# Kernel tuning notes

Measured on AMD Instinct MI355X. Metric: run time of the kernel, lower is better.

The kernel has to match this reference:

```python
import jax, jax.numpy as jnp
import numpy as np

B, C, H, W = 32, 512, 40, 40
NC = 20
STRIDE = 32
CONF_THRESH = 0.3
NMS_THRESH = 0.5


def setup_inputs() -> dict:
    key = jax.random.key(0)
    ks = jax.random.split(key, 7)
    # 0.02 scale on weights keeps sigmoid/exp in a realistic, non-saturated range
    return {
        "feat": jax.random.normal(ks[0], (B, C, H, W), dtype=jnp.float32),
        "w_obj": jax.random.normal(ks[1], (1, C), dtype=jnp.float32) * 0.02,
        "b_obj": jnp.zeros((1,), dtype=jnp.float32),
        "w_cls": jax.random.normal(ks[2], (NC, C), dtype=jnp.float32) * 0.02,
        "b_cls": jnp.zeros((NC,), dtype=jnp.float32),
        "w_reg": jax.random.normal(ks[3], (4, C), dtype=jnp.float32) * 0.02,
        "b_reg": jnp.zeros((4,), dtype=jnp.float32),
    }


def _pairwise_iou(b):  # b: [N,4] xyxy
    area = (b[:, 2] - b[:, 0]) * (b[:, 3] - b[:, 1])
    x1 = jnp.maximum(b[:, None, 0], b[None, :, 0])
    y1 = jnp.maximum(b[:, None, 1], b[None, :, 1])
    x2 = jnp.minimum(b[:, None, 2], b[None, :, 2])
    y2 = jnp.minimum(b[:, None, 3], b[None, :, 3])
    inter = jnp.maximum(x2 - x1, 0.0) * jnp.maximum(y2 - y1, 0.0)
    union = area[:, None] + area[None, :] - inter
    return inter / union


def _nms_single(boxes, scores, labels, conf_mask):
    # Greedy per-class NMS with fixed shapes (keep mask), matching the
    # original: suppression happens only among boxes of the same class
    # that pass conf_thresh, in descending score order.
    N = boxes.shape[0]
    order = jnp.argsort(-scores)
    b = boxes[order]
    l = labels[order]
    v = conf_mask[order]
    iou = _pairwise_iou(b)  # [N,N]
    idx = jnp.arange(N)
    later = idx[None, :] > idx[:, None]
    sup = (iou > NMS_THRESH) & (l[:, None] == l[None, :]) & later

    def body(i, keep):
        # if box i is still kept, suppress all later same-class overlaps
        return keep & ~(sup[i] & keep[i])

    keep_sorted = jax.lax.fori_loop(0, N, body, v)
    return jnp.zeros((N,), dtype=bool).at[order].set(keep_sorted)


def reference(feat, w_obj, b_obj, w_cls, b_cls, w_reg, b_reg):
    Bn, Cc, Hh, Ww = feat.shape
    N = Hh * Ww
    # permute(0,2,3,1).flatten(1,2) -> [B, H*W, C]
    x = feat.transpose(0, 2, 3, 1).reshape(Bn, N, Cc)
    # 1x1 convs == per-cell linear layers
    obj = jnp.einsum("bnc,oc->bno", x, w_obj) + b_obj  # [B,N,1]
    cls = jnp.einsum("bnc,oc->bno", x, w_cls) + b_cls  # [B,N,NC]
    reg = jnp.einsum("bnc,oc->bno", x, w_reg) + b_reg  # [B,N,4]
    # decode_boxes
    gy, gx = jnp.meshgrid(jnp.arange(Hh), jnp.arange(Ww), indexing="ij")
    grid = jnp.stack([gx, gy], axis=-1).reshape(-1, 2).astype(feat.dtype)  # [N,2]
    ctr = (jax.nn.sigmoid(reg[..., :2]) + grid) * STRIDE
    wh = jnp.exp(reg[..., 2:]) * STRIDE
    boxes = jnp.concatenate([ctr - wh * 0.5, ctr + wh * 0.5], axis=-1)  # [B,N,4]
    # scores = sqrt(sigmoid(obj) * sigmoid(cls)); per-cell best class
    sc = jnp.sqrt(jax.nn.sigmoid(obj) * jax.nn.sigmoid(cls))  # [B,N,NC]
    scores = sc.max(axis=-1)
    labels = jnp.argmax(sc, axis=-1)
    conf_mask = scores > CONF_THRESH
    keep = jax.vmap(_nms_single)(boxes, scores, labels, conf_mask)  # [B,N]
    out = jnp.concatenate(
        [jnp.where(keep[..., None], boxes, 0.0),
         jnp.where(keep, scores, 0.0)[..., None]],
        axis=-1,
    )  # [B,N,5]
    return out, labels, keep
```

## Files before the change

### kernel.cpp

```cpp
#include <hip/hip_runtime.h>
#include <stdint.h>
#include <stddef.h>

#define Bn 32
#define Cc 512
#define Hh 40
#define Ww 40
#define Npix 1600
#define NCx 20
#define NCELL (Bn*Npix)
#define CONF 0.3f
#define NMS_T 0.5f
#define NOUT 25
#define WSTRIDE 32

#define CB 64
#define BPI 25
#define NWAVE 4
#define CR (Cc/NWAVE)

#define WS_WPK    0
#define WS_BOXES  (WS_WPK + (size_t)Cc*WSTRIDE)
#define WS_SCORES (WS_BOXES + (size_t)NCELL*4)
#define WS_LABELS (WS_SCORES + (size_t)NCELL)

__device__ __forceinline__ float sigmoidf_(float x) {
    return 1.0f / (1.0f + expf(-x));
}

__global__ __launch_bounds__(64) void k0_pack(
    const float* __restrict__ w_obj, const float* __restrict__ w_cls,
    const float* __restrict__ w_reg, float* __restrict__ Wpk)
{
    int c = blockIdx.x * 64 + threadIdx.x;
    if (c < Cc) {
        float* row = Wpk + (size_t)c * WSTRIDE;
        row[0] = w_obj[c];
        #pragma unroll
        for (int o = 0; o < NCx; ++o) row[1 + o] = w_cls[o * Cc + c];
        #pragma unroll
        for (int o = 0; o < 4; ++o)   row[21 + o] = w_reg[o * Cc + c];
        row[25] = 0.f; row[26] = 0.f; row[27] = 0.f;
        row[28] = 0.f; row[29] = 0.f; row[30] = 0.f; row[31] = 0.f;
    }
}

__global__ __launch_bounds__(256) void k1_fused(
    const float* __restrict__ feat, const float* __restrict__ Wpk,
    const float* __restrict__ b_obj, const float* __restrict__ b_cls,
    const float* __restrict__ b_reg,
    float* __restrict__ out, float* __restrict__ ws_boxes,
    float* __restrict__ ws_scores, int* __restrict__ ws_labels)
{
    __shared__ float red[NOUT][CB][5];

    const int tid = threadIdx.x;
    const int w   = __builtin_amdgcn_readfirstlane(tid >> 6);
    const int l   = tid & 63;
    const int b   = blockIdx.x / BPI;
    const int j   = blockIdx.x % BPI;
    const int n0  = j * CB;

    float acc[NOUT];
    #pragma unroll
    for (int o = 0; o < NOUT; ++o) acc[o] = 0.f;

    const int cw0 = w * CR;
    {
        const float* fp  = feat + (size_t)b * (Cc * Npix) + (size_t)cw0 * Npix + (n0 + l);
        const float* wr0 = Wpk + (size_t)cw0 * WSTRIDE;
        #pragma unroll 4
        for (int cc = 0; cc < CR; ++cc) {
            float x = fp[(size_t)cc * Npix];
            const float4* wq = (const float4*)(wr0 + cc * WSTRIDE);
            #pragma unroll
            for (int q = 0; q < 6; ++q) {
                float4 wv = wq[q];
                const int ob = q * 4;
                acc[ob+0] = fmaf(x, wv.x, acc[ob+0]);
                acc[ob+1] = fmaf(x, wv.y, acc[ob+1]);
                acc[ob+2] = fmaf(x, wv.z, acc[ob+2]);
                acc[ob+3] = fmaf(x, wv.w, acc[ob+3]);
            }
            float4 wv6 = wq[6];
            acc[24] = fmaf(x, wv6.x, acc[24]);
        }
        #pragma unroll
        for (int o = 0; o < NOUT; ++o) red[o][l][w] = acc[o];
    }
    __syncthreads();

    if (tid < CB) {
        float v[NOUT];
        #pragma unroll
        for (int o = 0; o < NOUT; ++o) v[o] = red[o][tid][0];
        #pragma unroll
        for (int ch = 1; ch < NWAVE; ++ch) {
            #pragma unroll
            for (int o = 0; o < NOUT; ++o) v[o] += red[o][tid][ch];
        }

        float obj = v[0] + b_obj[0];
        float m = -1e30f; int label = 0;
        #pragma unroll
        for (int o = 0; o < NCx; ++o) {
            float cv = v[1 + o] + b_cls[o];
            if (cv > m) { m = cv; label = o; }
        }
        float r0 = v[21] + b_reg[0], r1 = v[22] + b_reg[1];
        float r2 = v[23] + b_reg[2], r3 = v[24] + b_reg[3];

        int n = n0 + tid;
        int g = b * Npix + n;
        int gy = n / Ww, gx = n % Ww;
        float cx = (sigmoidf_(r0) + (float)gx) * 32.0f;
        float cy = (sigmoidf_(r1) + (float)gy) * 32.0f;
        float bw = expf(r2) * 32.0f;
        float bh = expf(r3) * 32.0f;
        float x1 = cx - bw * 0.5f, y1 = cy - bh * 0.5f;
        float x2 = cx + bw * 0.5f, y2 = cy + bh * 0.5f;
        float score = sqrtf(sigmoidf_(obj) * sigmoidf_(m));

        ((float4*)ws_boxes)[g] = make_float4(x1, y1, x2, y2);
        ws_scores[g] = score;
        ws_labels[g] = label;

        float* orow = out + (size_t)g * 5;
        orow[0] = 0.f; orow[1] = 0.f; orow[2] = 0.f; orow[3] = 0.f; orow[4] = 0.f;
        out[(size_t)NCELL * 5 + g] = (float)label;
        out[(size_t)NCELL * 6 + g] = 0.f;
    }
}

#define KSUP 320
#define WUMAX ((KSUP + 31) / 32)

__global__ __launch_bounds__(256) void k3_nms(
    const float4* __restrict__ ws_boxes, const float* __restrict__ ws_scores,
    const int* __restrict__ ws_labels, float* __restrict__ out)
{
    __shared__ unsigned int cnt;
    __shared__ unsigned long long keys[2048];
    __shared__ float bx1[Npix], by1[Npix], bx2[Npix], by2[Npix], bar[Npix];
    __shared__ unsigned int sup[KSUP * WUMAX];
    __shared__ unsigned int keepbits[WUMAX];

    const int tid = threadIdx.x;
    const int b   = blockIdx.x / NCx;
    const int cls = blockIdx.x % NCx;
    const int gbase = b * Npix;

    if (tid == 0) cnt = 0;
    __syncthreads();

    for (int n = tid; n < Npix; n += 256) {
        float s = ws_scores[gbase + n];
        if (s > CONF && ws_labels[gbase + n] == cls) {
            unsigned int pos = atomicAdd(&cnt, 1u);
            unsigned int sb = __float_as_uint(s);
            keys[pos] = ((unsigned long long)(~sb) << 32) | (unsigned int)n;
        }
    }
    __syncthreads();
    const int k = (int)cnt;
    if (k == 0) return;

    int M = 2; while (M < k) M <<= 1;
    for (int s = tid; s < M; s += 256) if (s >= k) keys[s] = ~0ull;
    __syncthreads();

    for (int sz = 2; sz <= M; sz <<= 1) {
        for (int st = sz >> 1; st > 0; st >>= 1) {
            for (int t = tid; t < M; t += 256) {
                int p = t ^ st;
                if (p > t) {
                    unsigned long long a = keys[t], c = keys[p];
                    bool up = ((t & sz) == 0);
                    if (up ? (a > c) : (a < c)) { keys[t] = c; keys[p] = a; }
                }
            }
            __syncthreads();
        }
    }

    for (int s = tid; s < k; s += 256) {
        int n = (int)(unsigned int)keys[s];
        float4 bx = ws_boxes[gbase + n];
        bx1[s] = bx.x; by1[s] = bx.y; bx2[s] = bx.z; by2[s] = bx.w;
        bar[s] = (bx.z - bx.x) * (bx.w - bx.y);
    }
    __syncthreads();

    if (k <= KSUP) {
        const int wu = (k + 31) >> 5;
        for (int t = tid; t < k * wu; t += 256) {
            int i = t / wu, w = t - (t / wu) * wu;
            unsigned int bits = 0;
            int j0 = w << 5;
            float xi1 = bx1[i], yi1 = by1[i], xi2 = bx2[i], yi2 = by2[i], ai = bar[i];
            for (int jj = 0; jj < 32; ++jj) {
                int j = j0 + jj;
                if (j > i && j < k) {
                    float xx1 = fmaxf(xi1, bx1[j]);
                    float yy1 = fmaxf(yi1, by1[j]);
                    float xx2 = fminf(xi2, bx2[j]);
                    float yy2 = fminf(yi2, by2[j]);
                    float inter = fmaxf(xx2 - xx1, 0.f) * fmaxf(yy2 - yy1, 0.f);
                    float uni = ai + bar[j] - inter;
                    if (inter / uni > NMS_T) bits |= (1u << jj);
                }
            }
            sup[i * wu + w] = bits;
        }
        if (tid < wu) {
            int rem = k - (tid << 5);
            keepbits[tid] = (rem >= 32) ? 0xFFFFFFFFu : ((1u << rem) - 1u);
        }
        __syncthreads();

        if (tid < 64) {
            for (int i = 0; i < k; ++i) {
                unsigned int cur = keepbits[i >> 5];
                if ((cur >> (i & 31)) & 1u) {
                    if (tid < wu) keepbits[tid] &= ~sup[i * wu + tid];
                }
            }
            unsigned int* keepF = sup;
            for (int s2 = tid; s2 < k; s2 += 64)
                keepF[s2] = (keepbits[s2 >> 5] >> (s2 & 31)) & 1u;
        }
        __syncthreads();
    } else {
        unsigned int* keepF = sup;
        for (int s = tid; s < k; s += 256) keepF[s] = 1u;
        __syncthreads();
        for (int i = 0; i < k; ++i) {
            __syncthreads();
            if (keepF[i]) {
                float xi1 = bx1[i], yi1 = by1[i], xi2 = bx2[i], yi2 = by2[i], ai = bar[i];
                for (int j = i + 1 + tid; j < k; j += 256) {
                    float xx1 = fmaxf(xi1, bx1[j]);
                    float yy1 = fmaxf(yi1, by1[j]);
                    float xx2 = fminf(xi2, bx2[j]);
                    float yy2 = fminf(yi2, by2[j]);
                    float inter = fmaxf(xx2 - xx1, 0.f) * fmaxf(yy2 - yy1, 0.f);
                    float uni = ai + bar[j] - inter;
                    if (inter / uni > NMS_T) keepF[j] = 0u;
                }
            }
        }
        __syncthreads();
    }

    unsigned int* keepF = sup;
    for (int s = tid; s < k; s += 256) {
        if (keepF[s]) {
            int n = (int)(unsigned int)keys[s];
            unsigned int sb = ~(unsigned int)(keys[s] >> 32);
            float sc = __uint_as_float(sb);
            float* orow = out + (size_t)(gbase + n) * 5;
            orow[0] = bx1[s]; orow[1] = by1[s];
            orow[2] = bx2[s]; orow[3] = by2[s];
            orow[4] = sc;
            out[(size_t)NCELL * 6 + gbase + n] = 1.0f;
        }
    }
}

extern "C" void kernel_launch(void* const* d_in, const int* in_sizes, int n_in,
                              void* d_out, int out_size, void* d_ws, size_t ws_size,
                              hipStream_t stream) {
    const float* feat  = (const float*)d_in[0];
    const float* w_obj = (const float*)d_in[1];
    const float* b_obj = (const float*)d_in[2];
    const float* w_cls = (const float*)d_in[3];
    const float* b_cls = (const float*)d_in[4];
    const float* w_reg = (const float*)d_in[5];
    const float* b_reg = (const float*)d_in[6];
    float* out = (float*)d_out;
    float* ws  = (float*)d_ws;

    float* Wpk    = ws + WS_WPK;
    float* boxes  = ws + WS_BOXES;
    float* scores = ws + WS_SCORES;
    int*   labels = (int*)(ws + WS_LABELS);

    k0_pack<<<(Cc + 63) / 64, 64, 0, stream>>>(w_obj, w_cls, w_reg, Wpk);
    k1_fused<<<Bn * BPI, 256, 0, stream>>>(feat, Wpk, b_obj, b_cls, b_reg,
                                           out, boxes, scores, labels);
    k3_nms<<<Bn * NCx, 256, 0, stream>>>((const float4*)boxes, scores, labels, out);
}
```

Baseline: 220.7 us.

## Preload all feature channels into registers and use output-major weight layout

The weight pack is changed from a per-channel row of 32 floats to an output-major [25][512] layout. The projection kernel now loads all 128 channel values for its pixel into registers up front, then computes the 25 outputs in five passes of five accumulators each. The shared reduction buffer is reordered to [wave][out][pixel]. The aim is to issue all feature loads at once for more memory-level parallelism, at the cost of heavy register pressure (128 values held), which may lower occupancy or cause spills.

```diff
diff --git a/kernel.cpp b/kernel.cpp
--- a/kernel.cpp
+++ b/kernel.cpp
@@ -12,15 +12,14 @@
 #define CONF 0.3f
 #define NMS_T 0.5f
 #define NOUT 25
-#define WSTRIDE 32
 
 #define CB 64
 #define BPI 25
 #define NWAVE 4
 #define CR (Cc/NWAVE)
 
-#define WS_WPK    0
-#define WS_BOXES  (WS_WPK + (size_t)Cc*WSTRIDE)
+#define WS_WT     0
+#define WS_BOXES  (WS_WT + (size_t)NOUT*Cc)
 #define WS_SCORES (WS_BOXES + (size_t)NCELL*4)
 #define WS_LABELS (WS_SCORES + (size_t)NCELL)
 
@@ -30,29 +29,26 @@
 
 __global__ __launch_bounds__(64) void k0_pack(
     const float* __restrict__ w_obj, const float* __restrict__ w_cls,
-    const float* __restrict__ w_reg, float* __restrict__ Wpk)
+    const float* __restrict__ w_reg, float* __restrict__ Wt)
 {
     int c = blockIdx.x * 64 + threadIdx.x;
     if (c < Cc) {
-        float* row = Wpk + (size_t)c * WSTRIDE;
-        row[0] = w_obj[c];
-        #pragma unroll
-        for (int o = 0; o < NCx; ++o) row[1 + o] = w_cls[o * Cc + c];
-        #pragma unroll
-        for (int o = 0; o < 4; ++o)   row[21 + o] = w_reg[o * Cc + c];
-        row[25] = 0.f; row[26] = 0.f; row[27] = 0.f;
-        row[28] = 0.f; row[29] = 0.f; row[30] = 0.f; row[31] = 0.f;
+        Wt[c] = w_obj[c];
+        #pragma unroll
+        for (int o = 0; o < NCx; ++o) Wt[(size_t)(1 + o) * Cc + c] = w_cls[o * Cc + c];
+        #pragma unroll
+        for (int o = 0; o < 4; ++o)   Wt[(size_t)(21 + o) * Cc + c] = w_reg[o * Cc + c];
     }
 }
 
 __global__ __launch_bounds__(256) void k1_fused(
-    const float* __restrict__ feat, const float* __restrict__ Wpk,
+    const float* __restrict__ feat, const float* __restrict__ Wt,
     const float* __restrict__ b_obj, const float* __restrict__ b_cls,
     const float* __restrict__ b_reg,
     float* __restrict__ out, float* __restrict__ ws_boxes,
     float* __restrict__ ws_scores, int* __restrict__ ws_labels)
 {
-    __shared__ float red[NOUT][CB][5];
+    __shared__ float red[NWAVE][NOUT][CB];
 
     const int tid = threadIdx.x;
     const int w   = __builtin_amdgcn_readfirstlane(tid >> 6);
@@ -61,43 +57,47 @@
     const int j   = blockIdx.x % BPI;
     const int n0  = j * CB;
 
-    float acc[NOUT];
-    #pragma unroll
-    for (int o = 0; o < NOUT; ++o) acc[o] = 0.f;
-
-    const int cw0 = w * CR;
     {
-        const float* fp  = feat + (size_t)b * (Cc * Npix) + (size_t)cw0 * Npix + (n0 + l);
-        const float* wr0 = Wpk + (size_t)cw0 * WSTRIDE;
-        #pragma unroll 4
-        for (int cc = 0; cc < CR; ++cc) {
-            float x = fp[(size_t)cc * Npix];
-            const float4* wq = (const float4*)(wr0 + cc * WSTRIDE);
+        const float* fp = feat + (size_t)b * (Cc * Npix) + (size_t)(w * CR) * Npix + (n0 + l);
+        float x[CR];
+        #pragma unroll
+        for (int cc = 0; cc < CR; ++cc) x[cc] = fp[(size_t)cc * Npix];
+
+        const float* wt0 = Wt + w * CR;
+        #pragma unroll
+        for (int q = 0; q < 5; ++q) {
+            const float* w0 = wt0 + (size_t)(5 * q + 0) * Cc;
+            const float* w1 = wt0 + (size_t)(5 * q + 1) * Cc;
+            const float* w2 = wt0 + (size_t)(5 * q + 2) * Cc;
+            const float* w3 = wt0 + (size_t)(5 * q + 3) * Cc;
+            const float* w4 = wt0 + (size_t)(5 * q + 4) * Cc;
+            float a0 = 0.f, a1 = 0.f, a2 = 0.f, a3 = 0.f, a4 = 0.f;
             #pragma unroll
-            for (int q = 0; q < 6; ++q) {
-                float4 wv = wq[q];
-                const int ob = q * 4;
-                acc[ob+0] = fmaf(x, wv.x, acc[ob+0]);
-                acc[ob+1] = fmaf(x, wv.y, acc[ob+1]);
-                acc[ob+2] = fmaf(x, wv.z, acc[ob+2]);
-                acc[ob+3] = fmaf(x, wv.w, acc[ob+3]);
-            }
-            float4 wv6 = wq[6];
-            acc[24] = fmaf(x, wv6.x, acc[24]);
-        }
-        #pragma unroll
-        for (int o = 0; o < NOUT; ++o) red[o][l][w] = acc[o];
+            for (int cc = 0; cc < CR; ++cc) {
+                float xv = x[cc];
+                a0 = fmaf(xv, w0[cc], a0);
+                a1 = fmaf(xv, w1[cc], a1);
+                a2 = fmaf(xv, w2[cc], a2);
+                a3 = fmaf(xv, w3[cc], a3);
+                a4 = fmaf(xv, w4[cc], a4);
+            }
+            red[w][5 * q + 0][l] = a0;
+            red[w][5 * q + 1][l] = a1;
+            red[w][5 * q + 2][l] = a2;
+            red[w][5 * q + 3][l] = a3;
+            red[w][5 * q + 4][l] = a4;
+        }
     }
     __syncthreads();
 
     if (tid < CB) {
         float v[NOUT];
         #pragma unroll
-        for (int o = 0; o < NOUT; ++o) v[o] = red[o][tid][0];
+        for (int o = 0; o < NOUT; ++o) v[o] = red[0][o][tid];
         #pragma unroll
         for (int ch = 1; ch < NWAVE; ++ch) {
             #pragma unroll
-            for (int o = 0; o < NOUT; ++o) v[o] += red[o][tid][ch];
+            for (int o = 0; o < NOUT; ++o) v[o] += red[ch][o][tid];
         }
 
         float obj = v[0] + b_obj[0];
@@ -280,13 +280,13 @@
     float* out = (float*)d_out;
     float* ws  = (float*)d_ws;
 
-    float* Wpk    = ws + WS_WPK;
+    float* Wt     = ws + WS_WT;
     float* boxes  = ws + WS_BOXES;
     float* scores = ws + WS_SCORES;
     int*   labels = (int*)(ws + WS_LABELS);
 
-    k0_pack<<<(Cc + 63) / 64, 64, 0, stream>>>(w_obj, w_cls, w_reg, Wpk);
-    k1_fused<<<Bn * BPI, 256, 0, stream>>>(feat, Wpk, b_obj, b_cls, b_reg,
+    k0_pack<<<(Cc + 63) / 64, 64, 0, stream>>>(w_obj, w_cls, w_reg, Wt);
+    k1_fused<<<Bn * BPI, 256, 0, stream>>>(feat, Wt, b_obj, b_cls, b_reg,
                                            out, boxes, scores, labels);
     k3_nms<<<Bn * NCx, 256, 0, stream>>>((const float4*)boxes, scores, labels, out);
 }
```

Result: slower. 240.5 us (+9.0%).

## Stage packed weights in LDS and double-buffer feature loads in fused head

Applied to the files above, without the earlier changes.

The packed weight matrix is now copied into shared memory at block start and read from LDS instead of global/scalar memory. Feature loads are batched eight channels at a time with two register buffers, so the next group's global loads are in flight while the current group's FMAs run. The weight row stride shrinks from 32 to 28 floats to fit LDS, and the reduction buffer is laid out to reuse the same shared array. The cost is a 56KB LDS allocation per block, which limits occupancy, plus a redundant weight copy in every block.

```diff
diff --git a/kernel.cpp b/kernel.cpp
--- a/kernel.cpp
+++ b/kernel.cpp
@@ -12,17 +12,20 @@
 #define CONF 0.3f
 #define NMS_T 0.5f
 #define NOUT 25
-#define WSTRIDE 32
+#define WSTRIDE 28
 
 #define CB 64
 #define BPI 25
 #define NWAVE 4
 #define CR (Cc/NWAVE)
+#define FB 8
 
 #define WS_WPK    0
 #define WS_BOXES  (WS_WPK + (size_t)Cc*WSTRIDE)
 #define WS_SCORES (WS_BOXES + (size_t)NCELL*4)
 #define WS_LABELS (WS_SCORES + (size_t)NCELL)
+
+#define SMEM_FLOATS (Cc*WSTRIDE)
 
 __device__ __forceinline__ float sigmoidf_(float x) {
     return 1.0f / (1.0f + expf(-x));
@@ -41,7 +44,47 @@
         #pragma unroll
         for (int o = 0; o < 4; ++o)   row[21 + o] = w_reg[o * Cc + c];
         row[25] = 0.f; row[26] = 0.f; row[27] = 0.f;
-        row[28] = 0.f; row[29] = 0.f; row[30] = 0.f; row[31] = 0.f;
+    }
+}
+
+__device__ __forceinline__ void ld8(float dst[FB], const float* __restrict__ fp, int base) {
+    #pragma unroll
+    for (int t = 0; t < FB; ++t) dst[t] = fp[(size_t)(base + t) * Npix];
+}
+
+__device__ __forceinline__ void fma8_lds(float acc[NOUT], const float x[FB],
+                                         const float* __restrict__ wl, int base) {
+    #pragma unroll
+    for (int t = 0; t < FB; ++t) {
+        const float4* wr = (const float4*)(wl + (size_t)(base + t) * WSTRIDE);
+        float xv = x[t];
+        float4 w0 = wr[0], w1 = wr[1], w2 = wr[2], w3 = wr[3], w4 = wr[4], w5 = wr[5];
+        float4 w6 = wr[6];
+        acc[0]  = fmaf(xv, w0.x, acc[0]);
+        acc[1]  = fmaf(xv, w0.y, acc[1]);
+        acc[2]  = fmaf(xv, w0.z, acc[2]);
+        acc[3]  = fmaf(xv, w0.w, acc[3]);
+        acc[4]  = fmaf(xv, w1.x, acc[4]);
+        acc[5]  = fmaf(xv, w1.y, acc[5]);
+        acc[6]  = fmaf(xv, w1.z, acc[6]);
+        acc[7]  = fmaf(xv, w1.w, acc[7]);
+        acc[8]  = fmaf(xv, w2.x, acc[8]);
+        acc[9]  = fmaf(xv, w2.y, acc[9]);
+        acc[10] = fmaf(xv, w2.z, acc[10]);
+        acc[11] = fmaf(xv, w2.w, acc[11]);
+        acc[12] = fmaf(xv, w3.x, acc[12]);
+        acc[13] = fmaf(xv, w3.y, acc[13]);
+        acc[14] = fmaf(xv, w3.z, acc[14]);
+        acc[15] = fmaf(xv, w3.w, acc[15]);
+        acc[16] = fmaf(xv, w4.x, acc[16]);
+        acc[17] = fmaf(xv, w4.y, acc[17]);
+        acc[18] = fmaf(xv, w4.z, acc[18]);
+        acc[19] = fmaf(xv, w4.w, acc[19]);
+        acc[20] = fmaf(xv, w5.x, acc[20]);
+        acc[21] = fmaf(xv, w5.y, acc[21]);
+        acc[22] = fmaf(xv, w5.z, acc[22]);
+        acc[23] = fmaf(xv, w5.w, acc[23]);
+        acc[24] = fmaf(xv, w6.x, acc[24]);
     }
 }
 
@@ -52,7 +95,7 @@
     float* __restrict__ out, float* __restrict__ ws_boxes,
     float* __restrict__ ws_scores, int* __restrict__ ws_labels)
 {
-    __shared__ float red[NOUT][CB][5];
+    __shared__ float smem[SMEM_FLOATS];
 
     const int tid = threadIdx.x;
     const int w   = __builtin_amdgcn_readfirstlane(tid >> 6);
@@ -61,43 +104,58 @@
     const int j   = blockIdx.x % BPI;
     const int n0  = j * CB;
 
+    {
+        const float4* src = (const float4*)Wpk;
+        float4* dst = (float4*)smem;
+        #pragma unroll
+        for (int i = 0; i < SMEM_FLOATS / 4 / 256; ++i)
+            dst[tid + i * 256] = src[tid + i * 256];
+    }
+    __syncthreads();
+
     float acc[NOUT];
     #pragma unroll
     for (int o = 0; o < NOUT; ++o) acc[o] = 0.f;
 
-    const int cw0 = w * CR;
     {
-        const float* fp  = feat + (size_t)b * (Cc * Npix) + (size_t)cw0 * Npix + (n0 + l);
-        const float* wr0 = Wpk + (size_t)cw0 * WSTRIDE;
-        #pragma unroll 4
-        for (int cc = 0; cc < CR; ++cc) {
-            float x = fp[(size_t)cc * Npix];
-            const float4* wq = (const float4*)(wr0 + cc * WSTRIDE);
-            #pragma unroll
-            for (int q = 0; q < 6; ++q) {
-                float4 wv = wq[q];
-                const int ob = q * 4;
-                acc[ob+0] = fmaf(x, wv.x, acc[ob+0]);
-                acc[ob+1] = fmaf(x, wv.y, acc[ob+1]);
-                acc[ob+2] = fmaf(x, wv.z, acc[ob+2]);
-                acc[ob+3] = fmaf(x, wv.w, acc[ob+3]);
-            }
-            float4 wv6 = wq[6];
-            acc[24] = fmaf(x, wv6.x, acc[24]);
-        }
-        #pragma unroll
-        for (int o = 0; o < NOUT; ++o) red[o][l][w] = acc[o];
+        const int c0 = w * CR;
+        const float* fp = feat + (size_t)b * (Cc * Npix) + (size_t)c0 * Npix + (n0 + l);
+        const float* wl = smem + (size_t)c0 * WSTRIDE;
+
+        float xa[FB], xb[FB];
+        ld8(xa, fp, 0);
+        int base = 0;
+        #pragma unroll
+        for (int g = 0; g < CR / (2 * FB) - 1; ++g) {
+            ld8(xb, fp, base + FB);
+            fma8_lds(acc, xa, wl, base);
+            ld8(xa, fp, base + 2 * FB);
+            fma8_lds(acc, xb, wl, base + FB);
+            base += 2 * FB;
+        }
+        ld8(xb, fp, base + FB);
+        fma8_lds(acc, xa, wl, base);
+        fma8_lds(acc, xb, wl, base + FB);
+    }
+    __syncthreads();
+
+    {
+        float* red = smem;
+        #pragma unroll
+        for (int o = 0; o < NOUT; ++o) red[((w * NOUT) + o) * CB + l] = acc[o];
     }
     __syncthreads();
 
     if (tid < CB) {
+        const float* red = smem;
         float v[NOUT];
         #pragma unroll
-        for (int o = 0; o < NOUT; ++o) v[o] = red[o][tid][0];
+        for (int o = 0; o < NOUT; ++o) v[o] = red[o * CB + tid];
         #pragma unroll
         for (int ch = 1; ch < NWAVE; ++ch) {
             #pragma unroll
-            for (int o = 0; o < NOUT; ++o) v[o] += red[o][tid][ch];
+            for (int o = 0; o < NOUT; ++o)
+                v[o] += red[((ch * NOUT) + o) * CB + tid];
         }
 
         float obj = v[0] + b_obj[0];
```

After: 222.4 us. About the same (+0.8%).
